# Kernel optimization log

Measured on AMD Instinct MI355X. Metric: run time of the kernel, lower is better.

The kernel has to match this reference:

```python
import jax, jax.numpy as jnp
import numpy as np

B, NHID = 8192, 512
NUM_NODES, NUM_CLASSES = 50000, 40
K = 40
EPS = 1e-5


def _l2_normalize(x, axis=1):
    # matches torch F.normalize: x / max(||x||, 1e-12)
    n = jnp.sqrt(jnp.sum(x * x, axis=axis, keepdims=True))
    return x / jnp.maximum(n, 1e-12)


def setup_inputs() -> dict:
    key = jax.random.key(0)
    k1, k2, k3, k4 = jax.random.split(key, 4)
    return {
        "feat_output": jax.random.normal(k1, (B, NHID), dtype=jnp.float32),
        "cls_output": jax.random.normal(k2, (B, NUM_CLASSES), dtype=jnp.float32),
        "mem_fea": jax.random.uniform(k3, (NUM_NODES, NHID), dtype=jnp.float32),
        "mem_cls": jax.random.uniform(k4, (NUM_NODES, NUM_CLASSES), dtype=jnp.float32),
    }


def reference(feat_output, cls_output, mem_fea, mem_cls):
    # --- IM loss: entropy + diversity ---
    softmax_out = jax.nn.softmax(cls_output, axis=1)
    entropy_loss = jnp.mean(-jnp.sum(softmax_out * jnp.log(softmax_out + EPS), axis=1))
    mean_softmax = jnp.mean(softmax_out, axis=0)
    div_loss = jnp.sum(mean_softmax * jnp.log(mean_softmax + EPS))
    im_loss = entropy_loss + div_loss

    # --- KNN pseudo-labels from memory bank ---
    feat_norm = _l2_normalize(feat_output, axis=1)          # [B, nhid]
    mem_norm = _l2_normalize(mem_fea, axis=1)               # [N, nhid]
    sim = feat_norm @ mem_norm.T                            # [B, N]
    _, idx = jax.lax.top_k(sim, K + 1)                      # [B, K+1]
    idx_near = idx[:, 1:]                                   # drop self / top-1, [B, K]
    neigh_cls = mem_cls[idx_near]                           # [B, K, C]
    preds = jnp.argmax(jnp.mean(neigh_cls, axis=1), axis=1) # [B]

    # --- cross entropy with pseudo labels ---
    logp = jax.nn.log_softmax(cls_output, axis=1)
    cls_loss = -jnp.mean(jnp.take_along_axis(logp, preds[:, None], axis=1))

    return im_loss + cls_loss
```

## Files before the change

kernel.cpp:

```cpp
#include <hip/hip_runtime.h>
#include <hip/hip_bf16.h>

#define NB      8192
#define NHID    512
#define NN      50000
#define NC      40
#define KSEL    41
#define NCHUNK  4
#define CHUNK   12500
#define NTILES4 391
#define NTILES1 1563
#define EPS_F   1e-5f
#define BCAP    56
#define BTRIG   24

typedef __attribute__((ext_vector_type(8))) short  short8;
typedef __attribute__((ext_vector_type(4))) float  floatx4;

#define OFF_INVN 0u
#define OFF_LSE  200704u
#define OFF_PVAL 233472u
#define OFF_PIDX 5607424u
#define OFF_ACC  10981376u
#define WS_NEED  10981568u
#define OFF_MEMB 10981632u
#define WS_BF16_NEED (10981632u + 51200000u)

__device__ __forceinline__ unsigned pkbf(float x, float y) {
    union { __hip_bfloat162 b; unsigned u; } c;
    c.b = __float22bfloat162_rn(make_float2(x, y));
    return c.u;
}
__device__ __forceinline__ int simgt(float av, int ai, float bv, int bi) {
    return (av > bv || (av == bv && ai < bi)) ? 1 : 0;
}

__global__ void k_init(float* __restrict__ acc) {
    int t = threadIdx.x;
    if (t < 48) acc[t] = 0.f;
}

__global__ __launch_bounds__(256) void k_cls(const float* __restrict__ cls,
                                             float* __restrict__ lse,
                                             float* __restrict__ acc) {
    __shared__ float cacc[NC];
    __shared__ float entacc;
    int t = threadIdx.x;
    if (t == 0) entacc = 0.f;
    if (t < NC) cacc[t] = 0.f;
    __syncthreads();
    int row = blockIdx.x * 256 + t;
    float x[NC];
#pragma unroll
    for (int c = 0; c < NC; c++) x[c] = cls[row * NC + c];
    float m = x[0];
#pragma unroll
    for (int c = 1; c < NC; c++) m = fmaxf(m, x[c]);
    float S = 0.f;
#pragma unroll
    for (int c = 0; c < NC; c++) { float e = expf(x[c] - m); x[c] = e; S += e; }
    if (lse) lse[row] = m + logf(S);
    float inv = 1.f / S, ent = 0.f;
#pragma unroll
    for (int c = 0; c < NC; c++) {
        float p = x[c] * inv;
        ent += p * logf(p + EPS_F);
        atomicAdd(&cacc[c], p);
    }
    for (int off = 32; off; off >>= 1) ent += __shfl_xor(ent, off);
    if ((t & 63) == 0) atomicAdd(&entacc, ent);
    __syncthreads();
    if (t == 0) atomicAdd(&acc[0], entacc);
    if (t < NC) atomicAdd(&acc[2 + t], cacc[t]);
}

__global__ void k_final(const float* __restrict__ acc, float* __restrict__ out) {
    if (threadIdx.x == 0) {
        float ent = -acc[0] / (float)NB;
        float cl  = -acc[1] / (float)NB;
        float div = 0.f;
        for (int c = 0; c < NC; c++) {
            float msm = acc[2 + c] / (float)NB;
            div += msm * logf(msm + EPS_F);
        }
        out[0] = ent + div + cl;
    }
}


__global__ __launch_bounds__(256) void k_invnorm(const float* __restrict__ mem,
                                                 float* __restrict__ invn) {
    int w = threadIdx.x >> 6, lane = threadIdx.x & 63;
    int row = blockIdx.x * 4 + w;
    const float* p = mem + (size_t)row * NHID + lane * 8;
    float4 a = *(const float4*)p;
    float4 b = *(const float4*)(p + 4);
    float s = a.x * a.x + a.y * a.y + a.z * a.z + a.w * a.w
            + b.x * b.x + b.y * b.y + b.z * b.z + b.w * b.w;
    for (int off = 32; off; off >>= 1) s += __shfl_xor(s, off);
    if (lane == 0) invn[row] = 1.f / fmaxf(sqrtf(s), 1e-12f);
}

__global__ __launch_bounds__(256) void k_memcvt(const float* __restrict__ mem,
                                                unsigned short* __restrict__ memb) {
    size_t base = ((size_t)blockIdx.x * 256 + threadIdx.x) * 16;
    const float* s = mem + base;
    float4 a = *(const float4*)s;
    float4 b = *(const float4*)(s + 4);
    float4 c = *(const float4*)(s + 8);
    float4 d = *(const float4*)(s + 12);
    uint4 p0, p1;
    p0.x = pkbf(a.x, a.y); p0.y = pkbf(a.z, a.w);
    p0.z = pkbf(b.x, b.y); p0.w = pkbf(b.z, b.w);
    p1.x = pkbf(c.x, c.y); p1.y = pkbf(c.z, c.w);
    p1.z = pkbf(d.x, d.y); p1.w = pkbf(d.z, d.w);
    *(uint4*)(memb + base)     = p0;
    *(uint4*)(memb + base + 8) = p1;
}

template <bool BF16WS>
__global__ __launch_bounds__(256, 2) void k_gemm_topk4(
        const float* __restrict__ feat,
        const float* __restrict__ mem,
        const unsigned short* __restrict__ memb,
        const float* __restrict__ invn,
        float* __restrict__ pval, int* __restrict__ pidx) {
    __shared__ __align__(16) unsigned short Bbuf[32][520];
    __shared__ float simbuf[64][33];
    __shared__ float invs[32];
    __shared__ float bufval[64][BCAP];
    __shared__ unsigned short bufidx[64][BCAP];
    __shared__ float swv[4][KSEL];
    __shared__ int   swi[4][KSEL];

    const int tid  = threadIdx.x;
    const int lane = tid & 63;
    const int w    = tid >> 6;
    const int quad = lane >> 4;
    const int l16  = lane & 15;
    const int col  = lane & 31;
    const int half = lane >> 5;
    const int mbase  = blockIdx.x * 64;
    const int chunk  = blockIdx.y;
    const int nstart = chunk * CHUNK;

    short8 afrag[16];
    {
        const float* ar = feat + (size_t)(mbase + w * 16 + l16) * NHID + quad * 8;
#pragma unroll
        for (int s = 0; s < 16; s++) {
            float4 a = *(const float4*)(ar + s * 32);
            float4 b = *(const float4*)(ar + s * 32 + 4);
            union { unsigned u[4]; short8 s8; } fa;
            fa.u[0] = pkbf(a.x, a.y); fa.u[1] = pkbf(a.z, a.w);
            fa.u[2] = pkbf(b.x, b.y); fa.u[3] = pkbf(b.z, b.w);
            afrag[s] = fa.s8;
        }
    }

    float tval[16]; int tidx[16]; float theta[16]; int cnt[16];
#pragma unroll
    for (int r = 0; r < 16; r++) {
        tval[r] = -INFINITY; tidx[r] = 0x7fffffff; theta[r] = -INFINITY; cnt[r] = 0;
    }

    auto compact = [&](int R, float& tv, int& ti, float& th, int& c) {
        if (lane < KSEL) { swv[w][lane] = -INFINITY; swi[w][lane] = 0x7fffffff; }
        float v0 = -INFINITY; int i0 = 0x7fffffff;
        if (lane < c) { v0 = bufval[R][lane]; i0 = nstart + (int)bufidx[R][lane]; }
        int rr_ = 0, r0 = 0;
        for (int t2 = 0; t2 < c; t2++) {
            float bv = bufval[R][t2];
            int   bi = nstart + (int)bufidx[R][t2];
            rr_ += simgt(bv, bi, tv, ti);
            r0  += simgt(bv, bi, v0, i0);
        }
#pragma unroll
        for (int t2 = 0; t2 < KSEL; t2++) {
            float bv = __shfl(tv, t2);
            int   bi = __shfl(ti, t2);
            rr_ += simgt(bv, bi, tv, ti);
            r0  += simgt(bv, bi, v0, i0);
        }
        asm volatile("s_waitcnt lgkmcnt(0)" ::: "memory");
        if (rr_ < KSEL)              { swv[w][rr_] = tv; swi[w][rr_] = ti; }
        if (r0  < KSEL && lane < c)  { swv[w][r0]  = v0; swi[w][r0]  = i0; }
        asm volatile("s_waitcnt lgkmcnt(0)" ::: "memory");
        float nv = -INFINITY; int ni = 0x7fffffff;
        if (lane < KSEL) { nv = swv[w][lane]; ni = swi[w][lane]; }
        tv = nv; ti = ni;
        th = swv[w][KSEL - 1];
        c = 0;
    };

    for (int t = 0; t < NTILES4; t++) {
        __syncthreads();
        const int rbase = nstart + t * 32;
#pragma unroll
        for (int s = 0; s < 8; s++) {
            int id = tid + s * 256;
            int rl = id >> 6, ck = id & 63;
            int rg = rbase + rl; if (rg > NN - 1) rg = NN - 1;
            if (BF16WS) {
                *(uint4*)&Bbuf[rl][ck * 8] = *(const uint4*)(memb + (size_t)rg * NHID + ck * 8);
            } else {
                const float* src = mem + (size_t)rg * NHID + ck * 8;
                float4 a = *(const float4*)src;
                float4 b = *(const float4*)(src + 4);
                uint4 pk;
                pk.x = pkbf(a.x, a.y); pk.y = pkbf(a.z, a.w);
                pk.z = pkbf(b.x, b.y); pk.w = pkbf(b.z, b.w);
                *(uint4*)&Bbuf[rl][ck * 8] = pk;
            }
        }
        if (tid < 32) { int rg = rbase + tid; invs[tid] = invn[rg > NN - 1 ? NN - 1 : rg]; }
        __syncthreads();

        floatx4 acc0 = {0.f, 0.f, 0.f, 0.f}, acc1 = {0.f, 0.f, 0.f, 0.f};
#pragma unroll
        for (int s = 0; s < 16; s++) {
            short8 b0 = *(const short8*)&Bbuf[l16][s * 32 + quad * 8];
            short8 b1 = *(const short8*)&Bbuf[16 + l16][s * 32 + quad * 8];
            acc0 = __builtin_amdgcn_mfma_f32_16x16x32_bf16(afrag[s], b0, acc0, 0, 0, 0);
            acc1 = __builtin_amdgcn_mfma_f32_16x16x32_bf16(afrag[s], b1, acc1, 0, 0, 0);
        }
#pragma unroll
        for (int r = 0; r < 4; r++) {
            simbuf[w * 16 + quad * 4 + r][l16]      = acc0[r];
            simbuf[w * 16 + quad * 4 + r][16 + l16] = acc1[r];
        }

        int lim = CHUNK - t * 32; if (lim > 32) lim = 32;
        float inv_c = invs[col];
        const int relbase = t * 32;
#pragma unroll
        for (int p = 0; p < 8; p++) {
            const int myrow = w * 16 + p + (half << 3);
            float v = -INFINITY;
            if (col < lim) v = simbuf[myrow][col] * inv_c;
            float th = half ? theta[p + 8] : theta[p];
            unsigned long long mk = __ballot(v > th);
            unsigned mlo = (unsigned)mk;
            unsigned mhi = (unsigned)(mk >> 32);
            if (mlo) {
                if (!half && ((mlo >> col) & 1u)) {
                    int pos = cnt[p] + __popc(mlo & ((1u << col) - 1u));
                    bufval[w * 16 + p][pos] = v;
                    bufidx[w * 16 + p][pos] = (unsigned short)(relbase + col);
                }
                cnt[p] += __popc(mlo);
            }
            if (mhi) {
                if (half && ((mhi >> col) & 1u)) {
                    int pos = cnt[p + 8] + __popc(mhi & ((1u << col) - 1u));
                    bufval[w * 16 + p + 8][pos] = v;
                    bufidx[w * 16 + p + 8][pos] = (unsigned short)(relbase + col);
                }
                cnt[p + 8] += __popc(mhi);
            }
            if (cnt[p] > BTRIG)
                compact(w * 16 + p, tval[p], tidx[p], theta[p], cnt[p]);
            if (cnt[p + 8] > BTRIG)
                compact(w * 16 + p + 8, tval[p + 8], tidx[p + 8], theta[p + 8], cnt[p + 8]);
        }
    }

    const int g0 = mbase + w * 16;
#pragma unroll
    for (int p = 0; p < 16; p++) {
        if (cnt[p] > 0)
            compact(w * 16 + p, tval[p], tidx[p], theta[p], cnt[p]);
        if (lane < KSEL) {
            int base = ((g0 + p) * NCHUNK + chunk) * KSEL;
            pval[base + lane] = tval[p];
            pidx[base + lane] = tidx[p];
        }
    }
}

__global__ __launch_bounds__(256) void k_merge(
        const float* __restrict__ pval, const int* __restrict__ pidx,
        const float* __restrict__ memcls,
        const float* __restrict__ cls,
        const float* __restrict__ lse, float* __restrict__ acc) {
    __shared__ float cv[4][NCHUNK * KSEL];
    __shared__ int   ci[4][NCHUNK * KSEL];
    __shared__ int   sel[4][40];
    __shared__ float blksum;
    const int w = threadIdx.x >> 6, lane = threadIdx.x & 63;
    const int row = blockIdx.x * 4 + w;
    const int NCAND = NCHUNK * KSEL;
    if (threadIdx.x == 0) blksum = 0.f;
    if (lane < 40) sel[w][lane] = 0;
#pragma unroll
    for (int s = 0; s < 3; s++) {
        int i = lane + 64 * s;
        if (i < NCAND) { cv[w][i] = pval[(size_t)row * NCAND + i]; ci[w][i] = pidx[(size_t)row * NCAND + i]; }
    }
    __syncthreads();
#pragma unroll
    for (int s = 0; s < 3; s++) {
        int i = lane + 64 * s;
        if (i < NCAND) {
            float v = cv[w][i]; int id = ci[w][i];
            int rank = 0;
            for (int t = 0; t < NCAND; t++) {
                float tv = cv[w][t]; int ti = ci[w][t];
                if (tv > v || (tv == v && ti < id)) rank++;
            }
            if (rank >= 1 && rank <= 40) sel[w][rank - 1] = id;
        }
    }
    __syncthreads();
    float sv = -INFINITY; int scls = lane;
    if (lane < NC) {
        float s2 = 0.f;
        for (int j = 0; j < 40; j++) {
            int idx = sel[w][j];
            idx = idx < 0 ? 0 : (idx > NN - 1 ? NN - 1 : idx);
            s2 += memcls[(size_t)idx * NC + lane];
        }
        sv = s2;
    }
    for (int off = 32; off; off >>= 1) {
        float ov = __shfl_xor(sv, off);
        int   oc = __shfl_xor(scls, off);
        if (ov > sv || (ov == sv && oc < scls)) { sv = ov; scls = oc; }
    }
    if (lane == 0) atomicAdd(&blksum, cls[(size_t)row * NC + scls] - lse[row]);
    __syncthreads();
    if (threadIdx.x == 0) atomicAdd(&acc[1], blksum);
}

__global__ __launch_bounds__(256) void k_gemm_topk1(
        const float* __restrict__ feat,
        const float* __restrict__ mem,
        const float* __restrict__ cls,
        const float* __restrict__ memcls,
        float* __restrict__ acc) {
    __shared__ __align__(16) unsigned short Bbuf[32][520];
    __shared__ float simbuf[32][33];
    __shared__ float lvals[32][KSEL];
    __shared__ int   lidx[32][KSEL];
    __shared__ float invs[32];
    __shared__ float nrm8[32][8];
    __shared__ int   sel[4][40];
    __shared__ float blksum;

    const int tid  = threadIdx.x;
    const int lane = tid & 63;
    const int w    = tid >> 6;
    const int quad = lane >> 4;
    const int l16  = lane & 15;
    const int rowhalf = w & 1, colhalf = w >> 1;
    const int mbase = blockIdx.x * 32;

    short8 afrag[16];
    {
        const float* ar = feat + (size_t)(mbase + rowhalf * 16 + l16) * NHID + quad * 8;
#pragma unroll
        for (int s = 0; s < 16; s++) {
            float4 a = *(const float4*)(ar + s * 32);
            float4 b = *(const float4*)(ar + s * 32 + 4);
            union { unsigned u[4]; short8 s8; } fa;
            fa.u[0] = pkbf(a.x, a.y); fa.u[1] = pkbf(a.z, a.w);
            fa.u[2] = pkbf(b.x, b.y); fa.u[3] = pkbf(b.z, b.w);
            afrag[s] = fa.s8;
        }
    }

    if (tid < 32) {
        for (int i = 0; i < KSEL; i++) { lvals[tid][i] = -INFINITY; lidx[tid][i] = 0x7fffffff; }
    }
    if (tid == 0) blksum = 0.f;
    if (lane < 40) sel[w][lane] = 0;
    const bool owner = ((tid >> 3) & 7) == 0;
    const int  orow  = (tid >> 6) * 8 + (tid & 7);
    float minv = -INFINITY; int mini = 0x7fffffff; int minp = 0;

    for (int t = 0; t < NTILES1; t++) {
        __syncthreads();
        const int rbase = t * 32;
#pragma unroll
        for (int s = 0; s < 8; s++) {
            int id = tid + s * 256;
            int rl = id >> 6, ck = id & 63;
            int rg = rbase + rl; if (rg > NN - 1) rg = NN - 1;
            const float* src = mem + (size_t)rg * NHID + ck * 8;
            float4 a = *(const float4*)src;
            float4 b = *(const float4*)(src + 4);
            uint4 pk;
            pk.x = pkbf(a.x, a.y); pk.y = pkbf(a.z, a.w);
            pk.z = pkbf(b.x, b.y); pk.w = pkbf(b.z, b.w);
            *(uint4*)&Bbuf[rl][ck * 8] = pk;
        }
        __syncthreads();
        {
            int r = tid >> 3, p = tid & 7;
            int rg = rbase + r; if (rg > NN - 1) rg = NN - 1;
            const float* bp = mem + (size_t)rg * NHID + p * 64;
            float s = 0.f;
#pragma unroll
            for (int j = 0; j < 16; j++) {
                float4 v = *(const float4*)(bp + j * 4);
                s += v.x * v.x + v.y * v.y + v.z * v.z + v.w * v.w;
            }
            nrm8[r][p] = s;
        }
        __syncthreads();
        if (tid < 32) {
            float s = 0.f;
#pragma unroll
            for (int p = 0; p < 8; p++) s += nrm8[tid][p];
            invs[tid] = 1.f / fmaxf(sqrtf(s), 1e-12f);
        }
        floatx4 c4 = {0.f, 0.f, 0.f, 0.f};
#pragma unroll
        for (int s = 0; s < 16; s++) {
            short8 b = *(const short8*)&Bbuf[colhalf * 16 + l16][s * 32 + quad * 8];
            c4 = __builtin_amdgcn_mfma_f32_16x16x32_bf16(afrag[s], b, c4, 0, 0, 0);
        }
#pragma unroll
        for (int r = 0; r < 4; r++)
            simbuf[rowhalf * 16 + quad * 4 + r][colhalf * 16 + l16] = c4[r];
        __syncthreads();

        if (owner) {
            int lim = NN - rbase; if (lim > 32) lim = 32;
            for (int c = 0; c < lim; c++) {
                float v = simbuf[orow][c] * invs[c];
                if (v > minv) {
                    lvals[orow][minp] = v; lidx[orow][minp] = rbase + c;
                    minv = INFINITY; mini = -1;
                    for (int i = 0; i < KSEL; i++) {
                        float lv = lvals[orow][i]; int li = lidx[orow][i];
                        if (lv < minv || (lv == minv && li > mini)) { minv = lv; mini = li; minp = i; }
                    }
                }
            }
        }
    }
    __syncthreads();

    for (int it = 0; it < 8; it++) {
        const int r32 = it * 4 + w;
        const int grow = mbase + r32;
        if (lane < KSEL) {
            float v = lvals[r32][lane]; int id = lidx[r32][lane];
            int rank = 0;
            for (int j = 0; j < KSEL; j++) {
                float tv = lvals[r32][j]; int ti = lidx[r32][j];
                if (tv > v || (tv == v && ti < id)) rank++;
            }
            if (rank >= 1 && rank <= 40) sel[w][rank - 1] = id;
        }
        __syncthreads();
        float sv = -INFINITY; int scls = lane;
        if (lane < NC) {
            float s = 0.f;
            for (int j = 0; j < 40; j++) {
                int idx = sel[w][j];
                idx = idx < 0 ? 0 : (idx > NN - 1 ? NN - 1 : idx);
                s += memcls[(size_t)idx * NC + lane];
            }
            sv = s;
        }
        for (int off = 32; off; off >>= 1) {
            float ov = __shfl_xor(sv, off);
            int   oc = __shfl_xor(scls, off);
            if (ov > sv || (ov == sv && oc < scls)) { sv = ov; scls = oc; }
        }
        float x = (lane < NC) ? cls[(size_t)grow * NC + lane] : -INFINITY;
        float mx = x;
        for (int off = 32; off; off >>= 1) mx = fmaxf(mx, __shfl_xor(mx, off));
        float e = (lane < NC) ? expf(x - mx) : 0.f;
        float S = e;
        for (int off = 32; off; off >>= 1) S += __shfl_xor(S, off);
        float lse = mx + logf(S);
        float xp = __shfl(x, scls);
        if (lane == 0) atomicAdd(&blksum, xp - lse);
        __syncthreads();
    }
    if (tid == 0) atomicAdd(&acc[1], blksum);
}

extern "C" void kernel_launch(void* const* d_in, const int* in_sizes, int n_in,
                              void* d_out, int out_size, void* d_ws, size_t ws_size,
                              hipStream_t stream) {
    const float* feat = (const float*)d_in[0];
    const float* cls  = (const float*)d_in[1];
    const float* mem  = (const float*)d_in[2];
    const float* mcls = (const float*)d_in[3];
    float* out = (float*)d_out;
    char* ws = (char*)d_ws;

    if (ws_size >= (size_t)WS_NEED) {
        float* invn = (float*)(ws + OFF_INVN);
        float* lse  = (float*)(ws + OFF_LSE);
        float* pval = (float*)(ws + OFF_PVAL);
        int*   pidx = (int*)(ws + OFF_PIDX);
        float* acc  = (float*)(ws + OFF_ACC);
        k_init<<<1, 64, 0, stream>>>(acc);
        k_cls<<<NB / 256, 256, 0, stream>>>(cls, lse, acc);
        k_invnorm<<<NN / 4, 256, 0, stream>>>(mem, invn);
        if (ws_size >= (size_t)WS_BF16_NEED) {
            unsigned short* memb = (unsigned short*)(ws + OFF_MEMB);
            k_memcvt<<<(NN * NHID) / (256 * 16), 256, 0, stream>>>(mem, memb);
            k_gemm_topk4<true><<<dim3(NB / 64, NCHUNK), 256, 0, stream>>>(
                feat, mem, memb, invn, pval, pidx);
        } else {
            k_gemm_topk4<false><<<dim3(NB / 64, NCHUNK), 256, 0, stream>>>(
                feat, mem, nullptr, invn, pval, pidx);
        }
        k_merge<<<NB / 4, 256, 0, stream>>>(pval, pidx, mcls, cls, lse, acc);
        k_final<<<1, 64, 0, stream>>>(acc, out);
    } else {
        float* acc = (float*)ws;
        k_init<<<1, 64, 0, stream>>>(acc);
        k_cls<<<NB / 256, 256, 0, stream>>>(cls, nullptr, acc);
        k_gemm_topk1<<<NB / 32, 256, 0, stream>>>(feat, mem, cls, mcls, acc);
        k_final<<<1, 64, 0, stream>>>(acc, out);
    }
}
```

Before: 2.915 ms.

## Pipeline memory-tile staging with direct global-to-LDS loads and swizzled LDS layout

Restructures the fused GEMM plus top-k loop so the next 32-row memory tile is loaded into LDS while the current tile's similarities are filtered. In the bf16 path this uses global_load_lds direct copies, and the LDS tile uses an XOR-swizzled layout instead of padding. The inverse-norm value is prefetched into a register rather than through shared memory. The candidate buffer capacity and compaction trigger are lowered, and the per-row top-k state is seeded directly from the first tile instead of going through the ballot path. The aim is to hide global load latency behind the ballot/compaction work and cut LDS bank conflicts. In exchange it adds more synchronisation and depends on async LDS-DMA ordering and on the tile-0 seeding matching the compaction's index convention.

New measurement: 4.135 ms. 41.9% more time.

```diff
diff --git a/kernel.cpp b/kernel.cpp
--- a/kernel.cpp
+++ b/kernel.cpp
@@ -11,8 +11,8 @@
 #define NTILES4 391
 #define NTILES1 1563
 #define EPS_F   1e-5f
-#define BCAP    56
-#define BTRIG   24
+#define BCAP    48
+#define BTRIG   16
 
 typedef __attribute__((ext_vector_type(8))) short  short8;
 typedef __attribute__((ext_vector_type(4))) float  floatx4;
@@ -33,6 +33,11 @@
 }
 __device__ __forceinline__ int simgt(float av, int ai, float bv, int bi) {
     return (av > bv || (av == bv && ai < bi)) ? 1 : 0;
+}
+__device__ __forceinline__ void gl2lds16(const unsigned short* g, unsigned short* l) {
+    __builtin_amdgcn_global_load_lds(
+        (const __attribute__((address_space(1))) unsigned int*)g,
+        (__attribute__((address_space(3))) unsigned int*)l, 16, 0, 0);
 }
 
 __global__ void k_init(float* __restrict__ acc) {
@@ -125,9 +130,8 @@
         const unsigned short* __restrict__ memb,
         const float* __restrict__ invn,
         float* __restrict__ pval, int* __restrict__ pidx) {
-    __shared__ __align__(16) unsigned short Bbuf[32][520];
+    __shared__ __align__(16) unsigned short Bbuf[32 * 512];
     __shared__ float simbuf[64][33];
-    __shared__ float invs[32];
     __shared__ float bufval[64][BCAP];
     __shared__ unsigned short bufidx[64][BCAP];
     __shared__ float swv[4][KSEL];
@@ -193,34 +197,51 @@
         c = 0;
     };
 
-    for (int t = 0; t < NTILES4; t++) {
-        __syncthreads();
+    auto stage = [&](int t) {
         const int rbase = nstart + t * 32;
-#pragma unroll
-        for (int s = 0; s < 8; s++) {
-            int id = tid + s * 256;
-            int rl = id >> 6, ck = id & 63;
-            int rg = rbase + rl; if (rg > NN - 1) rg = NN - 1;
-            if (BF16WS) {
-                *(uint4*)&Bbuf[rl][ck * 8] = *(const uint4*)(memb + (size_t)rg * NHID + ck * 8);
-            } else {
+        if (BF16WS) {
+#pragma unroll
+            for (int j = 0; j < 8; j++) {
+                int r = w * 8 + j;
+                int rg = rbase + r; if (rg > NN - 1) rg = NN - 1;
+                const unsigned short* src =
+                    memb + (size_t)rg * NHID + ((lane ^ (r & 7)) * 8);
+                gl2lds16(src, &Bbuf[r * 512]);
+            }
+        } else {
+#pragma unroll
+            for (int s = 0; s < 8; s++) {
+                int id = tid + s * 256;
+                int rl = id >> 6, ck = id & 63;
+                int rg = rbase + rl; if (rg > NN - 1) rg = NN - 1;
                 const float* src = mem + (size_t)rg * NHID + ck * 8;
                 float4 a = *(const float4*)src;
                 float4 b = *(const float4*)(src + 4);
                 uint4 pk;
                 pk.x = pkbf(a.x, a.y); pk.y = pkbf(a.z, a.w);
                 pk.z = pkbf(b.x, b.y); pk.w = pkbf(b.z, b.w);
-                *(uint4*)&Bbuf[rl][ck * 8] = pk;
-            }
-        }
-        if (tid < 32) { int rg = rbase + tid; invs[tid] = invn[rg > NN - 1 ? NN - 1 : rg]; }
-        __syncthreads();
+                *(uint4*)&Bbuf[rl * 512 + (ck ^ (rl & 7)) * 8] = pk;
+            }
+        }
+    };
+    auto ldg_inv = [&](int t) -> float {
+        int rg = nstart + t * 32 + col; if (rg > NN - 1) rg = NN - 1;
+        return invn[rg];
+    };
+
+    stage(0);
+    float inv_nxt = ldg_inv(0);
+
+    for (int t = 0; t < NTILES4; t++) {
+        __syncthreads();
+        float inv_cur = inv_nxt;
 
         floatx4 acc0 = {0.f, 0.f, 0.f, 0.f}, acc1 = {0.f, 0.f, 0.f, 0.f};
 #pragma unroll
         for (int s = 0; s < 16; s++) {
-            short8 b0 = *(const short8*)&Bbuf[l16][s * 32 + quad * 8];
-            short8 b1 = *(const short8*)&Bbuf[16 + l16][s * 32 + quad * 8];
+            int g = 4 * s + quad;
+            short8 b0 = *(const short8*)&Bbuf[l16 * 512 + (g ^ (l16 & 7)) * 8];
+            short8 b1 = *(const short8*)&Bbuf[(16 + l16) * 512 + (g ^ (l16 & 7)) * 8];
             acc0 = __builtin_amdgcn_mfma_f32_16x16x32_bf16(afrag[s], b0, acc0, 0, 0, 0);
             acc1 = __builtin_amdgcn_mfma_f32_16x16x32_bf16(afrag[s], b1, acc1, 0, 0, 0);
         }
@@ -229,17 +250,27 @@
             simbuf[w * 16 + quad * 4 + r][l16]      = acc0[r];
             simbuf[w * 16 + quad * 4 + r][16 + l16] = acc1[r];
         }
+        __syncthreads();
+        if (t + 1 < NTILES4) {
+            stage(t + 1);
+            inv_nxt = ldg_inv(t + 1);
+        }
 
         int lim = CHUNK - t * 32; if (lim > 32) lim = 32;
-        float inv_c = invs[col];
         const int relbase = t * 32;
 #pragma unroll
         for (int p = 0; p < 8; p++) {
             const int myrow = w * 16 + p + (half << 3);
             float v = -INFINITY;
-            if (col < lim) v = simbuf[myrow][col] * inv_c;
+            if (col < lim) v = simbuf[myrow][col] * inv_cur;
+            if (t == 0) {
+                const int tr = p + (half << 3);
+                (void)tr;
+            }
             float th = half ? theta[p + 8] : theta[p];
-            unsigned long long mk = __ballot(v > th);
+            unsigned long long mk;
+            if (t == 0) mk = 0;
+            else        mk = __ballot(v > th);
             unsigned mlo = (unsigned)mk;
             unsigned mhi = (unsigned)(mk >> 32);
             if (mlo) {
@@ -262,6 +293,14 @@
                 compact(w * 16 + p, tval[p], tidx[p], theta[p], cnt[p]);
             if (cnt[p + 8] > BTRIG)
                 compact(w * 16 + p + 8, tval[p + 8], tidx[p + 8], theta[p + 8], cnt[p + 8]);
+        }
+        if (t == 0) {
+#pragma unroll
+            for (int r = 0; r < 16; r++) {
+                float v = -INFINITY;
+                if (lane < 32) v = simbuf[w * 16 + r][lane] * inv_cur;
+                if (lane < 32) { tval[r] = v; tidx[r] = nstart + lane; }
+            }
         }
     }
 
```
